# Performance work log

Measured on AMD Instinct MI355X. Metric: run time of the kernel, lower is better.

Reference implementation:

```python
import jax, jax.numpy as jnp
import numpy as np

B, D_IN = 8192, 1024
E, T = 8, 4
H1, H2, H3 = 1024, 512, 256


def setup_inputs() -> dict:
    key = jax.random.key(0)
    ks = jax.random.split(key, 8)
    s1 = 1.0 / np.sqrt(D_IN)
    s2 = 1.0 / np.sqrt(H1)
    s3 = 1.0 / np.sqrt(H2)
    return {
        "x": jax.random.normal(ks[0], (B, D_IN), jnp.float32),
        "W1": jax.random.normal(ks[1], (E, D_IN, H1), jnp.float32) * s1,
        "b1": jnp.zeros((E, H1), jnp.float32),
        "W2": jax.random.normal(ks[2], (E, H1, H2), jnp.float32) * s2,
        "b2": jnp.zeros((E, H2), jnp.float32),
        "W3": jax.random.normal(ks[3], (E, H2, H3), jnp.float32) * s3,
        "b3": jnp.zeros((E, H3), jnp.float32),
        "gate_w": jax.random.normal(ks[4], (D_IN, T * E), jnp.float32) * 0.05,
    }


def reference(x, W1, b1, W2, b2, W3, b3, gate_w):
    # Expert MLPs, vectorized over experts: h = relu(x @ W + b)
    h = jax.nn.relu(jnp.einsum("bi,eio->beo", x, W1) + b1[None])      # [B,E,H1]
    h = jax.nn.relu(jnp.einsum("beh,eho->beo", h, W2) + b2[None])     # [B,E,H2]
    h = jax.nn.relu(jnp.einsum("beh,eho->beo", h, W3) + b3[None])     # [B,E,H3]
    expert_outputs = jnp.transpose(h, (0, 2, 1))                       # [B,D_out,E]

    # Gates: logits [B, T*E] -> [B,T,E], softmax over experts, -> [B,E,T]
    logits = (x @ gate_w).reshape(B, T, E)
    gates = jax.nn.softmax(logits, axis=2)
    gates = jnp.transpose(gates, (0, 2, 1))                            # [B,E,T]

    mmoe_output = jnp.matmul(expert_outputs, gates)                    # [B,D_out,T]
    # unstack along task axis -> tuple of T [B, D_out] arrays
    return tuple(mmoe_output[:, :, t] for t in range(T))
```

## Files before the change

### kernel.cpp

```cpp
#include <hip/hip_runtime.h>


#define B_ROWS 8192
#define D_IN   1024
#define NEXP   8
#define NTASK  4
#define H1     1024
#define H2     512
#define H3     256

typedef __attribute__((ext_vector_type(8))) short bf16x8;
typedef __attribute__((ext_vector_type(4))) float f32x4;

__device__ __forceinline__ unsigned short f2bf(float f) {
    union { float f; unsigned int u; } x; x.f = f;
    unsigned int r = x.u + 0x7fffu + ((x.u >> 16) & 1u);
    return (unsigned short)(r >> 16);
}
__device__ __forceinline__ float bf2f(unsigned short u) {
    union { unsigned int u; float f; } x; x.u = ((unsigned int)u) << 16;
    return x.f;
}

__device__ __forceinline__ void gload_lds16(const void* gptr, void* lptr) {
    __builtin_amdgcn_global_load_lds(
        (__attribute__((address_space(1))) void*)gptr,
        (__attribute__((address_space(3))) void*)lptr,
        16, 0, 0);
}

struct __align__(8) us4 { unsigned short x, y, z, w; };

__global__ void transpose_convert_kernel(const float* __restrict__ W,
                                         unsigned short* __restrict__ Wt,
                                         int K, int N) {
    __shared__ float tile[64][65];
    const int e = blockIdx.z;
    const float* We = W + (size_t)e * K * N;
    unsigned short* Wte = Wt + (size_t)e * K * N;
    const int k0 = blockIdx.x * 64, n0 = blockIdx.y * 64;
    const int tid = threadIdx.x;
    const int tn = tid & 63;
    const int tk = tid >> 6;
#pragma unroll
    for (int i = 0; i < 16; ++i)
        tile[tk * 16 + i][tn] = We[(size_t)(k0 + tk * 16 + i) * N + n0 + tn];
    __syncthreads();
    const int wk = (tid & 15) * 4;
    const int wn = tid >> 4;
#pragma unroll
    for (int i = 0; i < 4; ++i) {
        const int n = wn + i * 16;
        us4 o;
        o.x = f2bf(tile[wk + 0][n]);
        o.y = f2bf(tile[wk + 1][n]);
        o.z = f2bf(tile[wk + 2][n]);
        o.w = f2bf(tile[wk + 3][n]);
        *(us4*)&Wte[(size_t)(n0 + n) * K + k0 + wk] = o;
    }
}

__global__ __launch_bounds__(256, 4) void gemm_bias_relu_kernel(
    const unsigned short* __restrict__ A, long long Aes,
    const unsigned short* __restrict__ Bt, long long Bes,
    const float* __restrict__ bias, long long bias_es,
    unsigned short* __restrict__ C, long long Ces,
    int M, int N, int K) {
    __shared__ __align__(16) unsigned short sA[128 * 64];
    __shared__ __align__(16) unsigned short sB[128 * 64];

    const int tid  = threadIdx.x;
    const int lane = tid & 63;
    const int w    = tid >> 6;
    const int wr   = w >> 1, wc = w & 1;
    const int quad = lane >> 4, l15 = lane & 15;
    const int r8   = lane >> 3;
    const int c8   = lane & 7;
    const int gchunk = c8 ^ r8;

    const unsigned int gy   = gridDim.y;
    const unsigned int lin  = blockIdx.x + gridDim.x * (blockIdx.y + gy * blockIdx.z);
    const unsigned int e    = lin & 7;
    const unsigned int slot = lin >> 3;
    const int gysh = __builtin_ctz(gy);
    const int n0 = (int)(slot & (gy - 1)) * 128;
    const int m0 = (int)(slot >> gysh) * 128;

    A    += (size_t)e * Aes;
    Bt   += (size_t)e * Bes;
    bias += (size_t)e * bias_es;
    C    += (size_t)e * Ces;

    const unsigned short* Abase = A + (size_t)(m0 + w * 32 + r8) * K + gchunk * 8;
    const unsigned short* Bbase = Bt + (size_t)(n0 + w * 32 + r8) * K + gchunk * 8;
    unsigned short* sAw = &sA[(w * 32 + r8) * 64 + c8 * 8];
    unsigned short* sBw = &sB[(w * 32 + r8) * 64 + c8 * 8];

    f32x4 acc[4][4] = {};
    const int swz = l15 & 7;

    for (int k0 = 0; k0 < K; k0 += 64) {
#pragma unroll
        for (int q = 0; q < 4; ++q) {
            gload_lds16(Abase + (size_t)(q * 8) * K + k0, sAw + q * 8 * 64);
            gload_lds16(Bbase + (size_t)(q * 8) * K + k0, sBw + q * 8 * 64);
        }
        __syncthreads();

#pragma unroll
        for (int s = 0; s < 2; ++s) {
            const int cs = ((s * 4 + quad) ^ swz) * 8;
            bf16x8 af[4], bfv[4];
#pragma unroll
            for (int i = 0; i < 4; ++i)
                af[i] = *(const bf16x8*)&sA[(wr * 64 + i * 16 + l15) * 64 + cs];
#pragma unroll
            for (int j = 0; j < 4; ++j)
                bfv[j] = *(const bf16x8*)&sB[(wc * 64 + j * 16 + l15) * 64 + cs];
#pragma unroll
            for (int i = 0; i < 4; ++i)
#pragma unroll
                for (int j = 0; j < 4; ++j)
                    acc[i][j] = __builtin_amdgcn_mfma_f32_16x16x32_bf16(
                        af[i], bfv[j], acc[i][j], 0, 0, 0);
        }
        __syncthreads();
    }

#pragma unroll
    for (int j = 0; j < 4; ++j) {
        const int col = n0 + wc * 64 + j * 16 + l15;
        const float bv = bias[col];
#pragma unroll
        for (int i = 0; i < 4; ++i) {
#pragma unroll
            for (int r = 0; r < 4; ++r) {
                const int row = m0 + wr * 64 + i * 16 + quad * 4 + r;
                float v = acc[i][j][r] + bv;
                v = v > 0.f ? v : 0.f;
                C[(size_t)row * N + col] = f2bf(v);
            }
        }
    }
}

__global__ void gates_convert_kernel(const float* __restrict__ x,
                                     const float* __restrict__ gw,
                                     float* __restrict__ gates,
                                     unsigned short* __restrict__ xb) {
    const int tid = threadIdx.x;
    const size_t base = (size_t)blockIdx.x * 8192 + (size_t)tid * 32;
#pragma unroll
    for (int i = 0; i < 8; ++i) {
        float4 v = *(const float4*)&x[base + i * 4];
        us4 o4;
        o4.x = f2bf(v.x); o4.y = f2bf(v.y); o4.z = f2bf(v.z); o4.w = f2bf(v.w);
        ((us4*)xb)[base / 4 + i] = o4;
    }
    const int o = tid & 31;
    const int r = tid >> 5;
    const int b = blockIdx.x * 8 + r;
    const float* xr = x + (size_t)b * D_IN;
    float acc = 0.f;
    for (int k = 0; k < D_IN; k += 4) {
        float4 xv = *(const float4*)&xr[k];
        acc += xv.x * gw[(k + 0) * 32 + o];
        acc += xv.y * gw[(k + 1) * 32 + o];
        acc += xv.z * gw[(k + 2) * 32 + o];
        acc += xv.w * gw[(k + 3) * 32 + o];
    }
    float m = acc;
    m = fmaxf(m, __shfl_xor(m, 1));
    m = fmaxf(m, __shfl_xor(m, 2));
    m = fmaxf(m, __shfl_xor(m, 4));
    float ex = __expf(acc - m);
    float s = ex;
    s += __shfl_xor(s, 1);
    s += __shfl_xor(s, 2);
    s += __shfl_xor(s, 4);
    gates[(size_t)b * 32 + o] = ex / s;
}

__global__ void combine_kernel(const unsigned short* __restrict__ h3,
                               const float* __restrict__ gates,
                               float* __restrict__ out) {
    __shared__ float g[32];
    const int b = blockIdx.x;
    const int d = threadIdx.x;
    if (d < 32) g[d] = gates[(size_t)b * 32 + d];
    __syncthreads();
    float acc[NTASK] = {0.f, 0.f, 0.f, 0.f};
#pragma unroll
    for (int e = 0; e < NEXP; ++e) {
        const float h = bf2f(h3[((size_t)e * B_ROWS + b) * H3 + d]);
#pragma unroll
        for (int t = 0; t < NTASK; ++t) acc[t] += h * g[t * 8 + e];
    }
#pragma unroll
    for (int t = 0; t < NTASK; ++t)
        out[((size_t)t * B_ROWS + b) * H3 + d] = acc[t];
}

#define OFF_XBF 0u
#define OFF_W1T 16777216u
#define OFF_W2T 33554432u
#define OFF_W3T 41943040u
#define OFF_G   44040192u
#define OFF_H1  45088768u
#define OFF_H2  179306496u
#define OFF_H3  45088768u

extern "C" void kernel_launch(void* const* d_in, const int* in_sizes, int n_in,
                              void* d_out, int out_size, void* d_ws, size_t ws_size,
                              hipStream_t stream) {
    const float* x  = (const float*)d_in[0];
    const float* W1 = (const float*)d_in[1];
    const float* b1 = (const float*)d_in[2];
    const float* W2 = (const float*)d_in[3];
    const float* b2 = (const float*)d_in[4];
    const float* W3 = (const float*)d_in[5];
    const float* b3 = (const float*)d_in[6];
    const float* gw = (const float*)d_in[7];
    float* out = (float*)d_out;
    char* ws = (char*)d_ws;

    unsigned short* xbf = (unsigned short*)(ws + OFF_XBF);
    unsigned short* w1t = (unsigned short*)(ws + OFF_W1T);
    unsigned short* w2t = (unsigned short*)(ws + OFF_W2T);
    unsigned short* w3t = (unsigned short*)(ws + OFF_W3T);
    float*          gts = (float*)(ws + OFF_G);
    unsigned short* h1  = (unsigned short*)(ws + OFF_H1);
    unsigned short* h2  = (unsigned short*)(ws + OFF_H2);
    unsigned short* h3  = (unsigned short*)(ws + OFF_H3);

    transpose_convert_kernel<<<dim3(D_IN / 64, H1 / 64, NEXP), dim3(256), 0, stream>>>(W1, w1t, D_IN, H1);
    transpose_convert_kernel<<<dim3(H1 / 64, H2 / 64, NEXP), dim3(256), 0, stream>>>(W2, w2t, H1, H2);
    transpose_convert_kernel<<<dim3(H2 / 64, H3 / 64, NEXP), dim3(256), 0, stream>>>(W3, w3t, H2, H3);
    gates_convert_kernel<<<dim3(B_ROWS / 8), dim3(256), 0, stream>>>(x, gw, gts, xbf);

    gemm_bias_relu_kernel<<<dim3(B_ROWS / 128, H1 / 128, NEXP), dim3(256), 0, stream>>>(
        xbf, 0LL,
        w1t, (long long)H1 * D_IN,
        b1, (long long)H1,
        h1, (long long)B_ROWS * H1,
        B_ROWS, H1, D_IN);
    gemm_bias_relu_kernel<<<dim3(B_ROWS / 128, H2 / 128, NEXP), dim3(256), 0, stream>>>(
        h1, (long long)B_ROWS * H1,
        w2t, (long long)H2 * H1,
        b2, (long long)H2,
        h2, (long long)B_ROWS * H2,
        B_ROWS, H2, H1);
    gemm_bias_relu_kernel<<<dim3(B_ROWS / 128, H3 / 128, NEXP), dim3(256), 0, stream>>>(
        h2, (long long)B_ROWS * H2,
        w3t, (long long)H3 * H2,
        b3, (long long)H3,
        h3, (long long)B_ROWS * H3,
        B_ROWS, H3, H2);

    combine_kernel<<<dim3(B_ROWS), dim3(256), 0, stream>>>(h3, gts, out);
}
```

Measured before the change: 449.7 us.

## Rewrite expert GEMM as 256x256 double-buffered pipelined kernel with 8 waves

Replaces the 128x128 single-buffered GEMM with a 256x256 tile kernel using 512 threads. It double-buffers LDS and splits each K-step into four MFMA phases, interleaving async global-to-LDS prefetch of the next tile with compute under raw barriers. It also raises MFMA wave priority and uses explicit vmcnt waits. The goal is to hide load latency and raise arithmetic intensity per tile. The cost is 128KB of LDS per block, larger register pressure, and fewer blocks for the smaller N=256 layer.

```diff
diff --git a/kernel.cpp b/kernel.cpp
--- a/kernel.cpp
+++ b/kernel.cpp
@@ -30,6 +30,15 @@
 }
 
 struct __align__(8) us4 { unsigned short x, y, z, w; };
+
+#define BAR() do {                                   \
+        asm volatile("" ::: "memory");               \
+        __builtin_amdgcn_s_barrier();                \
+        asm volatile("" ::: "memory");               \
+    } while (0)
+
+#define MFMA_BF16(a, b, c) \
+    __builtin_amdgcn_mfma_f32_16x16x32_bf16((a), (b), (c), 0, 0, 0)
 
 __global__ void transpose_convert_kernel(const float* __restrict__ W,
                                          unsigned short* __restrict__ Wt,
@@ -60,82 +69,174 @@
     }
 }
 
-__global__ __launch_bounds__(256, 4) void gemm_bias_relu_kernel(
+
+__device__ __forceinline__ void stage_half(const unsigned short* g,
+                                           unsigned short* s,
+                                           int h, int kt, int K, int tid) {
+    gload_lds16(g + (size_t)(h * 128) * K + kt * 64,
+                s + h * 8192 + tid * 8);
+    gload_lds16(g + (size_t)(h * 128 + 64) * K + kt * 64,
+                s + h * 8192 + 4096 + tid * 8);
+}
+
+template <bool PF1, bool PF2, int CKPT>
+__device__ __forceinline__ void tile8(
+    unsigned short* sAc, unsigned short* sBc,
+    unsigned short* sAn, unsigned short* sBn,
+    const unsigned short* gA, const unsigned short* gB,
+    int K, int tid, int aRow, int bRow, int ck0, int ck1,
+    int kt1, int kt2, f32x4 (&acc)[8][4]) {
+    bf16x8 af[4][2], b0[2][2], b1[2][2];
+
+#pragma unroll
+    for (int i = 0; i < 4; ++i) {
+        af[i][0] = *(const bf16x8*)&sAc[aRow + i * 16 * 64 + ck0];
+        af[i][1] = *(const bf16x8*)&sAc[aRow + i * 16 * 64 + ck1];
+    }
+#pragma unroll
+    for (int j = 0; j < 2; ++j) {
+        b0[j][0] = *(const bf16x8*)&sBc[bRow + j * 16 * 64 + ck0];
+        b0[j][1] = *(const bf16x8*)&sBc[bRow + j * 16 * 64 + ck1];
+    }
+    if (PF1) stage_half(gB, sBn, 1, kt1, K, tid);
+    BAR();
+    __builtin_amdgcn_s_setprio(1);
+#pragma unroll
+    for (int i = 0; i < 4; ++i)
+#pragma unroll
+        for (int j = 0; j < 2; ++j) {
+            acc[i][j] = MFMA_BF16(af[i][0], b0[j][0], acc[i][j]);
+            acc[i][j] = MFMA_BF16(af[i][1], b0[j][1], acc[i][j]);
+        }
+    __builtin_amdgcn_s_setprio(0);
+    BAR();
+
+#pragma unroll
+    for (int j = 0; j < 2; ++j) {
+        b1[j][0] = *(const bf16x8*)&sBc[bRow + (32 + j * 16) * 64 + ck0];
+        b1[j][1] = *(const bf16x8*)&sBc[bRow + (32 + j * 16) * 64 + ck1];
+    }
+    if (PF1) stage_half(gA, sAn, 1, kt1, K, tid);
+    BAR();
+    __builtin_amdgcn_s_setprio(1);
+#pragma unroll
+    for (int i = 0; i < 4; ++i)
+#pragma unroll
+        for (int j = 0; j < 2; ++j) {
+            acc[i][2 + j] = MFMA_BF16(af[i][0], b1[j][0], acc[i][2 + j]);
+            acc[i][2 + j] = MFMA_BF16(af[i][1], b1[j][1], acc[i][2 + j]);
+        }
+    __builtin_amdgcn_s_setprio(0);
+    BAR();
+
+#pragma unroll
+    for (int i = 0; i < 4; ++i) {
+        af[i][0] = *(const bf16x8*)&sAc[aRow + (64 + i * 16) * 64 + ck0];
+        af[i][1] = *(const bf16x8*)&sAc[aRow + (64 + i * 16) * 64 + ck1];
+    }
+    if (PF2) stage_half(gB, sBc, 0, kt2, K, tid);
+    BAR();
+    __builtin_amdgcn_s_setprio(1);
+#pragma unroll
+    for (int i = 0; i < 4; ++i)
+#pragma unroll
+        for (int j = 0; j < 2; ++j) {
+            acc[4 + i][2 + j] = MFMA_BF16(af[i][0], b1[j][0], acc[4 + i][2 + j]);
+            acc[4 + i][2 + j] = MFMA_BF16(af[i][1], b1[j][1], acc[4 + i][2 + j]);
+        }
+    __builtin_amdgcn_s_setprio(0);
+    BAR();
+
+    if (PF2) stage_half(gA, sAc, 0, kt2, K, tid);
+    BAR();
+    __builtin_amdgcn_s_setprio(1);
+#pragma unroll
+    for (int i = 0; i < 4; ++i)
+#pragma unroll
+        for (int j = 0; j < 2; ++j) {
+            acc[4 + i][j] = MFMA_BF16(af[i][0], b0[j][0], acc[4 + i][j]);
+            acc[4 + i][j] = MFMA_BF16(af[i][1], b0[j][1], acc[4 + i][j]);
+        }
+    __builtin_amdgcn_s_setprio(0);
+    if (CKPT == 4)      asm volatile("s_waitcnt vmcnt(4)" ::: "memory");
+    else if (CKPT == 0) asm volatile("s_waitcnt vmcnt(0)" ::: "memory");
+    BAR();
+}
+
+__global__ __launch_bounds__(512, 2) void gemm256_bias_relu_kernel(
     const unsigned short* __restrict__ A, long long Aes,
     const unsigned short* __restrict__ Bt, long long Bes,
     const float* __restrict__ bias, long long bias_es,
     unsigned short* __restrict__ C, long long Ces,
     int M, int N, int K) {
-    __shared__ __align__(16) unsigned short sA[128 * 64];
-    __shared__ __align__(16) unsigned short sB[128 * 64];
+    __shared__ __align__(16) unsigned short sA[2][16384];
+    __shared__ __align__(16) unsigned short sB[2][16384];
 
     const int tid  = threadIdx.x;
     const int lane = tid & 63;
     const int w    = tid >> 6;
-    const int wr   = w >> 1, wc = w & 1;
+    const int wm   = w >> 2;
+    const int wn   = w & 3;
     const int quad = lane >> 4, l15 = lane & 15;
-    const int r8   = lane >> 3;
-    const int c8   = lane & 7;
-    const int gchunk = c8 ^ r8;
+    const int swz  = l15 & 7;
+    const int srow = tid >> 3;
+    const int schk = tid & 7;
+    const int gchunk = schk ^ (srow & 7);
 
     const unsigned int gy   = gridDim.y;
     const unsigned int lin  = blockIdx.x + gridDim.x * (blockIdx.y + gy * blockIdx.z);
     const unsigned int e    = lin & 7;
     const unsigned int slot = lin >> 3;
     const int gysh = __builtin_ctz(gy);
-    const int n0 = (int)(slot & (gy - 1)) * 128;
-    const int m0 = (int)(slot >> gysh) * 128;
+    const int n0 = (int)(slot & (gy - 1)) * 256;
+    const int m0 = (int)(slot >> gysh) * 256;
 
     A    += (size_t)e * Aes;
     Bt   += (size_t)e * Bes;
     bias += (size_t)e * bias_es;
     C    += (size_t)e * Ces;
 
-    const unsigned short* Abase = A + (size_t)(m0 + w * 32 + r8) * K + gchunk * 8;
-    const unsigned short* Bbase = Bt + (size_t)(n0 + w * 32 + r8) * K + gchunk * 8;
-    unsigned short* sAw = &sA[(w * 32 + r8) * 64 + c8 * 8];
-    unsigned short* sBw = &sB[(w * 32 + r8) * 64 + c8 * 8];
-
-    f32x4 acc[4][4] = {};
-    const int swz = l15 & 7;
-
-    for (int k0 = 0; k0 < K; k0 += 64) {
-#pragma unroll
-        for (int q = 0; q < 4; ++q) {
-            gload_lds16(Abase + (size_t)(q * 8) * K + k0, sAw + q * 8 * 64);
-            gload_lds16(Bbase + (size_t)(q * 8) * K + k0, sBw + q * 8 * 64);
-        }
-        __syncthreads();
-
-#pragma unroll
-        for (int s = 0; s < 2; ++s) {
-            const int cs = ((s * 4 + quad) ^ swz) * 8;
-            bf16x8 af[4], bfv[4];
-#pragma unroll
-            for (int i = 0; i < 4; ++i)
-                af[i] = *(const bf16x8*)&sA[(wr * 64 + i * 16 + l15) * 64 + cs];
-#pragma unroll
-            for (int j = 0; j < 4; ++j)
-                bfv[j] = *(const bf16x8*)&sB[(wc * 64 + j * 16 + l15) * 64 + cs];
-#pragma unroll
-            for (int i = 0; i < 4; ++i)
-#pragma unroll
-                for (int j = 0; j < 4; ++j)
-                    acc[i][j] = __builtin_amdgcn_mfma_f32_16x16x32_bf16(
-                        af[i], bfv[j], acc[i][j], 0, 0, 0);
-        }
-        __syncthreads();
-    }
+    const unsigned short* gA = A  + (size_t)(m0 + srow) * K + gchunk * 8;
+    const unsigned short* gB = Bt + (size_t)(n0 + srow) * K + gchunk * 8;
+
+    f32x4 acc[8][4] = {};
+
+    stage_half(gB, sB[0], 0, 0, K, tid);
+    stage_half(gA, sA[0], 0, 0, K, tid);
+    stage_half(gB, sB[0], 1, 0, K, tid);
+    stage_half(gA, sA[0], 1, 0, K, tid);
+    stage_half(gB, sB[1], 0, 1, K, tid);
+    stage_half(gA, sA[1], 0, 1, K, tid);
+    asm volatile("s_waitcnt vmcnt(4)" ::: "memory");
+    BAR();
+
+    const int aRow = (wm * 128 + l15) * 64;
+    const int bRow = (wn * 64 + l15) * 64;
+    const int ck0  = ((0 + quad) ^ swz) * 8;
+    const int ck1  = ((4 + quad) ^ swz) * 8;
+    const int NT   = K >> 6;
+
+    int t = 0;
+    for (; t + 3 < NT; t += 2) {
+        tile8<true, true, 4>(sA[0], sB[0], sA[1], sB[1], gA, gB, K, tid,
+                             aRow, bRow, ck0, ck1, t + 1, t + 2, acc);
+        tile8<true, true, 4>(sA[1], sB[1], sA[0], sB[0], gA, gB, K, tid,
+                             aRow, bRow, ck0, ck1, t + 2, t + 3, acc);
+    }
+    tile8<true, false, 0>(sA[0], sB[0], sA[1], sB[1], gA, gB, K, tid,
+                          aRow, bRow, ck0, ck1, NT - 1, 0, acc);
+    tile8<false, false, -1>(sA[1], sB[1], sA[0], sB[0], gA, gB, K, tid,
+                            aRow, bRow, ck0, ck1, 0, 0, acc);
 
 #pragma unroll
     for (int j = 0; j < 4; ++j) {
-        const int col = n0 + wc * 64 + j * 16 + l15;
+        const int col = n0 + wn * 64 + j * 16 + l15;
         const float bv = bias[col];
 #pragma unroll
-        for (int i = 0; i < 4; ++i) {
+        for (int i = 0; i < 8; ++i) {
 #pragma unroll
             for (int r = 0; r < 4; ++r) {
-                const int row = m0 + wr * 64 + i * 16 + quad * 4 + r;
+                const int row = m0 + wm * 128 + i * 16 + quad * 4 + r;
                 float v = acc[i][j][r] + bv;
                 v = v > 0.f ? v : 0.f;
                 C[(size_t)row * N + col] = f2bf(v);
@@ -238,19 +339,19 @@
     transpose_convert_kernel<<<dim3(H2 / 64, H3 / 64, NEXP), dim3(256), 0, stream>>>(W3, w3t, H2, H3);
     gates_convert_kernel<<<dim3(B_ROWS / 8), dim3(256), 0, stream>>>(x, gw, gts, xbf);
 
-    gemm_bias_relu_kernel<<<dim3(B_ROWS / 128, H1 / 128, NEXP), dim3(256), 0, stream>>>(
+    gemm256_bias_relu_kernel<<<dim3(B_ROWS / 256, H1 / 256, NEXP), dim3(512), 0, stream>>>(
         xbf, 0LL,
         w1t, (long long)H1 * D_IN,
         b1, (long long)H1,
         h1, (long long)B_ROWS * H1,
         B_ROWS, H1, D_IN);
-    gemm_bias_relu_kernel<<<dim3(B_ROWS / 128, H2 / 128, NEXP), dim3(256), 0, stream>>>(
+    gemm256_bias_relu_kernel<<<dim3(B_ROWS / 256, H2 / 256, NEXP), dim3(512), 0, stream>>>(
         h1, (long long)B_ROWS * H1,
         w2t, (long long)H2 * H1,
         b2, (long long)H2,
         h2, (long long)B_ROWS * H2,
         B_ROWS, H2, H1);
-    gemm_bias_relu_kernel<<<dim3(B_ROWS / 128, H3 / 128, NEXP), dim3(256), 0, stream>>>(
+    gemm256_bias_relu_kernel<<<dim3(B_ROWS / 256, H3 / 256, NEXP), dim3(512), 0, stream>>>(
         h2, (long long)B_ROWS * H2,
         w3t, (long long)H3 * H2,
         b3, (long long)H3,
```

After: 525.6 us. 1.17x slower.
